# Performance work log

Hardware: AMD Instinct MI355X
Metric: run time of the kernel (lower is better)

The kernel has to match this reference:

```python
import jax, jax.numpy as jnp
import numpy as np

ALPHA = 4.0   # spikingjelly surrogate.Sigmoid default alpha
TAU = 2.0
HEADS = 8

@jax.custom_vjp
def spike_fn(x):
    return (x >= 0).astype(x.dtype)

def _spike_fwd(x):
    return spike_fn(x), x

def _spike_bwd(x, g):
    s = jax.nn.sigmoid(ALPHA * x)
    return (g * ALPHA * s * (1.0 - s),)

spike_fn.defvjp(_spike_fwd, _spike_bwd)

def lif(x, v_th=1.0):
    """Multi-step LIF over leading time axis. Hard reset to 0, detach_reset."""
    def step(v, xt):
        v = v + (xt - v) / TAU
        s = spike_fn(v - v_th)
        v = v * (1.0 - jax.lax.stop_gradient(s))
        return v, s
    _, spikes = jax.lax.scan(step, jnp.zeros_like(x[0]), x)
    return spikes

def conv1x1(x, w, b=None):
    # x: (T,B,C,H,W), w: (O,C) -> (T,B,O,H,W)
    y = jnp.einsum('tbchw,oc->tbohw', x, w)
    if b is not None:
        y = y + b[None, None, :, None, None]
    return y

def bn(x, gamma, beta, mean, var, eps=1e-5):
    inv = gamma / jnp.sqrt(var + eps)
    shift = beta - mean * inv
    return x * inv[None, None, :, None, None] + shift[None, None, :, None, None]

def setup_inputs() -> dict:
    key = jax.random.key(0)
    T, B, C, H, W = 4, 16, 512, 16, 16
    ks = jax.random.split(key, 24)
    def w(k):
        return jax.random.normal(k, (C, C), jnp.float32) * (1.0 / np.sqrt(C))
    def bn_params(k0, k1):
        g = 1.0 + 0.1 * jax.random.normal(k0, (C,), jnp.float32)
        b = 0.1 * jax.random.normal(k1, (C,), jnp.float32)
        m = 0.1 * jax.random.normal(jax.random.fold_in(k0, 7), (C,), jnp.float32)
        v = jax.random.uniform(jax.random.fold_in(k1, 7), (C,), jnp.float32, 0.5, 1.5)
        return g, b, m, v
    x = jax.random.normal(ks[0], (T, B, C, H, W), jnp.float32)
    q_g, q_b, q_m, q_v = bn_params(ks[4], ks[5])
    k_g, k_b, k_m, k_v = bn_params(ks[6], ks[7])
    v_g, v_b, v_m, v_v = bn_params(ks[8], ks[9])
    p_g, p_b2, p_m, p_v = bn_params(ks[10], ks[11])
    return {
        'x': x,
        'q_w': w(ks[1]), 'q_g': q_g, 'q_b': q_b, 'q_m': q_m, 'q_v': q_v,
        'k_w': w(ks[2]), 'k_g': k_g, 'k_b': k_b, 'k_m': k_m, 'k_v': k_v,
        'v_w': w(ks[3]), 'v_g': v_g, 'v_b': v_b, 'v_m': v_m, 'v_v': v_v,
        'proj_w': w(ks[12]),
        'proj_b': 0.1 * jax.random.normal(ks[13], (C,), jnp.float32),
        'p_g': p_g, 'p_b2': p_b2, 'p_m': p_m, 'p_v': p_v,
    }

def reference(x, q_w, q_g, q_b, q_m, q_v, k_w, k_g, k_b, k_m, k_v,
              v_w, v_g, v_b, v_m, v_v, proj_w, proj_b, p_g, p_b2, p_m, p_v):
    T, B, C, H, W = x.shape
    d = C // HEADS
    N = H * W
    identity = x
    xs = lif(x)  # shortcut_lif

    def to_heads(y):
        # (T,B,C,H,W) -> flatten(3) -> (T,B,C,N) -> (T,B,N,C) -> (T,B,N,h,d) -> (T,B,h,N,d)
        return y.reshape(T, B, C, N).transpose(0, 1, 3, 2).reshape(T, B, N, HEADS, d).transpose(0, 1, 3, 2, 4)

    q = to_heads(lif(bn(conv1x1(xs, q_w), q_g, q_b, q_m, q_v)))
    k = to_heads(lif(bn(conv1x1(xs, k_w), k_g, k_b, k_m, k_v)))
    v = to_heads(lif(bn(conv1x1(xs, v_w), v_g, v_b, v_m, v_v)))

    kv = (k * v).sum(axis=3, keepdims=True)        # (T,B,h,1,d) linear spike attention
    kv = lif(kv, v_th=0.5)                         # talking_heads_lif (conv1d never applied in source forward)
    attn = q * kv                                  # (T,B,h,N,d)

    y = attn.transpose(0, 1, 2, 4, 3).reshape(T, B, C, H, W)
    y = bn(conv1x1(y, proj_w, proj_b), p_g, p_b2, p_m, p_v)
    return y + identity
```

## Files before the change

kernel.cpp:

```cpp
#include <hip/hip_runtime.h>


#define T_  4
#define B_  16
#define C_  512
#define N_  256
#define O3_ 1536
#define EPS_ 1e-5f

typedef unsigned int uint32;

__global__ void k_prep(const float* __restrict__ qw, const float* __restrict__ kw,
                       const float* __restrict__ vw, const float* __restrict__ pw,
                       const float* qg,const float* qb,const float* qm,const float* qv,
                       const float* kg,const float* kb,const float* km,const float* kvr,
                       const float* vg,const float* vb,const float* vm,const float* vv,
                       const float* pg,const float* pb2,const float* pm,const float* pv,
                       const float* projb, const float* __restrict__ x,
                       float* __restrict__ wqkv_t, float* __restrict__ pwt,
                       float* __restrict__ bnc, uint32* __restrict__ xs_mask32,
                       uint32* __restrict__ cnt32){
    __shared__ float tile[64 * 65];
    __shared__ uint32 sm32[64 * 17];
    int bx = blockIdx.x, tid = threadIdx.x;
    if (bx < 256) {
        const float* src; float* dst; int ocol;
        int tl;
        if (bx < 192) { int g = bx / 64; tl = bx % 64;
            src = (g == 0) ? qw : (g == 1) ? kw : vw;
            dst = wqkv_t; ocol = g * 512;
        } else { tl = bx - 192; src = pw; dst = pwt; ocol = 0; }
        int o0 = (tl >> 3) * 64, c0 = (tl & 7) * 64;
        int dstride = (bx < 192) ? O3_ : C_;
        #pragma unroll
        for (int i = 0; i < 16; i++) {
            int idx = i * 256 + tid;
            int cl = idx & 63, ol = idx >> 6;
            tile[ol * 65 + cl] = src[(size_t)(o0 + ol) * C_ + c0 + cl];
        }
        __syncthreads();
        #pragma unroll
        for (int i = 0; i < 16; i++) {
            int idx = i * 256 + tid;
            int ol = idx & 63, cl = idx >> 6;
            dst[(size_t)(c0 + cl) * dstride + ocol + o0 + ol] = tile[ol * 65 + cl];
        }
    } else if (bx < 258) {
        int ch = (bx - 256) * 256 + tid;
        if (ch < C_) {
            {   float inv = qg[ch] / sqrtf(qv[ch] + EPS_);
                bnc[ch] = inv;            bnc[512 + ch]  = qb[ch] - qm[ch] * inv; }
            {   float inv = kg[ch] / sqrtf(kvr[ch] + EPS_);
                bnc[1024 + ch] = inv;     bnc[1536 + ch] = kb[ch] - km[ch] * inv; }
            {   float inv = vg[ch] / sqrtf(vv[ch] + EPS_);
                bnc[2048 + ch] = inv;     bnc[2560 + ch] = vb[ch] - vm[ch] * inv; }
            {   float inv = pg[ch] / sqrtf(pv[ch] + EPS_);
                float shift = pb2[ch] - pm[ch] * inv;
                bnc[3072 + ch] = inv;     bnc[3584 + ch] = projb[ch] * inv + shift; }
        }
    } else if (bx < 770) {
        int r = bx - 258;
        int b = r >> 5, rem = r & 31;
        int c0 = (rem >> 2) * 64, n0 = (rem & 3) * 64;
        #pragma unroll
        for (int i = 0; i < 4; i++) {
            int idx = i * 256 + tid;
            int nq = idx & 15, cl = idx >> 4;
            const float* xp = x + ((size_t)b * C_ + c0 + cl) * N_ + n0 + nq * 4;
            float4 xv[4];
            #pragma unroll
            for (int t = 0; t < 4; t++)
                xv[t] = *reinterpret_cast<const float4*>(xp + (size_t)t * B_ * C_ * N_);
            uint32 packed = 0;
            #pragma unroll
            for (int e = 0; e < 4; e++) {
                float v = 0.f; unsigned m = 0;
                #pragma unroll
                for (int t = 0; t < 4; t++) {
                    float xt = reinterpret_cast<const float*>(&xv[t])[e];
                    v = v + (xt - v) * 0.5f;
                    if (v - 1.0f >= 0.f) { m |= 1u << t; v = 0.f; }
                }
                packed |= m << (8 * e);
            }
            sm32[cl * 17 + nq] = packed;
        }
        __syncthreads();
        #pragma unroll
        for (int i = 0; i < 4; i++) {
            int idx = i * 256 + tid;
            int cq = idx & 15, nl = idx >> 4;
            uint32 outp = 0;
            #pragma unroll
            for (int e = 0; e < 4; e++) {
                uint32 wv = sm32[(cq * 4 + e) * 17 + (nl >> 2)];
                outp |= ((wv >> (8 * (nl & 3))) & 0xffu) << (8 * e);
            }
            xs_mask32[((size_t)b * N_ + n0 + nl) * 128 + (c0 >> 2) + cq] = outp;
        }
    } else {
        int idx = (bx - 770) * 256 + tid;
        cnt32[idx] = 0;
    }
}

__global__ __launch_bounds__(384) void
k2_qkv(const unsigned char* __restrict__ xs_mask,
       const float* __restrict__ wqkv_t,
       const float* __restrict__ bnc,
       unsigned char* __restrict__ q_mask,
       uint32* __restrict__ cnt32){
    __shared__ uint32 smask[128];
    __shared__ uint32 scnt;
    __shared__ uint32 slist[512];
    int n = blockIdx.x, b = blockIdx.y, tid = threadIdx.x;
    size_t colbase = ((size_t)b * N_ + n) * C_;
    if (tid < 128) smask[tid] = reinterpret_cast<const uint32*>(xs_mask + colbase)[tid];
    if (tid == 0) scnt = 0;
    __syncthreads();
    if (tid < 256) {
        const unsigned char* smb = (const unsigned char*)smask;
        #pragma unroll
        for (int h = 0; h < 2; h++) {
            int c = tid + (h << 8);
            unsigned m = smb[c];
            if (m) { unsigned p = atomicAdd(&scnt, 1u); slist[p] = (unsigned)c | (m << 16); }
        }
    }
    __syncthreads();
    int cnt = scnt;

    int g = tid >> 7;
    float acc[4][4];
    #pragma unroll
    for (int t = 0; t < 4; t++)
        #pragma unroll
        for (int i = 0; i < 4; i++) acc[t][i] = 0.f;

#define ACC4(t, w_) { acc[t][0]+=w_.x; acc[t][1]+=w_.y; acc[t][2]+=w_.z; acc[t][3]+=w_.w; }
    int j = 0;
    for (; j + 4 <= cnt; j += 4) {
        unsigned e0 = __builtin_amdgcn_readfirstlane(slist[j]);
        unsigned e1 = __builtin_amdgcn_readfirstlane(slist[j + 1]);
        unsigned e2 = __builtin_amdgcn_readfirstlane(slist[j + 2]);
        unsigned e3 = __builtin_amdgcn_readfirstlane(slist[j + 3]);
        float4 w0 = reinterpret_cast<const float4*>(wqkv_t + (size_t)(e0 & 0xffffu) * O3_)[tid];
        float4 w1 = reinterpret_cast<const float4*>(wqkv_t + (size_t)(e1 & 0xffffu) * O3_)[tid];
        float4 w2 = reinterpret_cast<const float4*>(wqkv_t + (size_t)(e2 & 0xffffu) * O3_)[tid];
        float4 w3 = reinterpret_cast<const float4*>(wqkv_t + (size_t)(e3 & 0xffffu) * O3_)[tid];
        unsigned m0 = e0 >> 16, m1 = e1 >> 16, m2 = e2 >> 16, m3 = e3 >> 16;
        if (m0 & 1u) ACC4(0, w0)  if (m0 & 2u) ACC4(1, w0)
        if (m0 & 4u) ACC4(2, w0)  if (m0 & 8u) ACC4(3, w0)
        if (m1 & 1u) ACC4(0, w1)  if (m1 & 2u) ACC4(1, w1)
        if (m1 & 4u) ACC4(2, w1)  if (m1 & 8u) ACC4(3, w1)
        if (m2 & 1u) ACC4(0, w2)  if (m2 & 2u) ACC4(1, w2)
        if (m2 & 4u) ACC4(2, w2)  if (m2 & 8u) ACC4(3, w2)
        if (m3 & 1u) ACC4(0, w3)  if (m3 & 2u) ACC4(1, w3)
        if (m3 & 4u) ACC4(2, w3)  if (m3 & 8u) ACC4(3, w3)
    }
    for (; j < cnt; j++) {
        unsigned e0 = __builtin_amdgcn_readfirstlane(slist[j]);
        float4 w0 = reinterpret_cast<const float4*>(wqkv_t + (size_t)(e0 & 0xffffu) * O3_)[tid];
        unsigned m0 = e0 >> 16;
        if (m0 & 1u) ACC4(0, w0)  if (m0 & 2u) ACC4(1, w0)
        if (m0 & 4u) ACC4(2, w0)  if (m0 & 8u) ACC4(3, w0)
    }
#undef ACC4

    int chb = (tid & 127) * 4;
    unsigned packed = 0;
    #pragma unroll
    for (int i = 0; i < 4; i++) {
        int ch = chb + i;
        float inv = bnc[g * 1024 + ch];
        float sh  = bnc[g * 1024 + 512 + ch];
        float v = 0.f; unsigned bits = 0;
        #pragma unroll
        for (int t = 0; t < 4; t++) {
            float pre = acc[t][i] * inv + sh;
            v = v + (pre - v) * 0.5f;
            if (v - 1.0f >= 0.f) { bits |= 1u << t; v = 0.f; }
        }
        packed |= bits << (8 * i);
    }
    if (g == 0)      reinterpret_cast<uint32*>(q_mask + colbase)[tid] = packed;
    else if (g == 1) smask[tid - 128] = packed;
    __syncthreads();
    if (g == 2) {
        unsigned kb = smask[tid - 256];
        unsigned kv = packed & kb;
        if (kv) {
            uint32* cbase = cnt32 + b * 1024 + (chb >> 1);
            #pragma unroll
            for (int t = 0; t < 4; t++) {
                unsigned v01 = ((kv >> t) & 1u) | (((kv >> (8 + t)) & 1u) << 16);
                unsigned v23 = ((kv >> (16 + t)) & 1u) | (((kv >> (24 + t)) & 1u) << 16);
                if (v01) atomicAdd(cbase + t * 256, v01);
                if (v23) atomicAdd(cbase + t * 256 + 1, v23);
            }
        }
    }
}

__global__ __launch_bounds__(256) void
k4_attn_proj(const unsigned char* __restrict__ q_mask,
             const uint32* __restrict__ cnt32,
             const float* __restrict__ pwt,
             const float* __restrict__ bnc,
             float* __restrict__ y_t){
    __shared__ uint32 smask[2][128];
    __shared__ uint32 scnt[2];
    __shared__ uint32 slist[2][512];
    int b = blockIdx.y, tid = threadIdx.x;
    int col = tid >> 7, ctid = tid & 127;
    int n = blockIdx.x * 2 + col;
    size_t colbase = ((size_t)b * N_ + n) * C_;
    unsigned kvs_packed = 0;
    {
        const uint32* cbase = cnt32 + b * 1024 + ctid * 2;
        uint32 c01[4], c23[4];
        #pragma unroll
        for (int t = 0; t < 4; t++) { c01[t] = cbase[t * 256]; c23[t] = cbase[t * 256 + 1]; }
        #pragma unroll
        for (int e = 0; e < 4; e++) {
            float v = 0.f; unsigned bits = 0;
            #pragma unroll
            for (int t = 0; t < 4; t++) {
                uint32 pair = (e < 2) ? c01[t] : c23[t];
                float cn = (float)(int)((e & 1) ? (pair >> 16) : (pair & 0xffffu));
                v = v + (cn - v) * 0.5f;
                if (v - 0.5f >= 0.f) { bits |= 1u << t; v = 0.f; }
            }
            kvs_packed |= bits << (8 * e);
        }
    }
    {
        uint32 qm = reinterpret_cast<const uint32*>(q_mask + colbase)[ctid];
        smask[col][ctid] = qm & kvs_packed;
    }
    if (ctid == 0) scnt[col] = 0;
    __syncthreads();
    {
        const unsigned char* smb = (const unsigned char*)smask[col];
        #pragma unroll
        for (int h = 0; h < 4; h++) {
            int c = ctid * 4 + h;
            unsigned m = smb[c];
            if (m) { unsigned p = atomicAdd(&scnt[col], 1u); slist[col][p] = (unsigned)c | (m << 16); }
        }
    }
    __syncthreads();
    int cnt = scnt[col];
    const uint32* lst = slist[col];

    float acc[4][4];
    #pragma unroll
    for (int t = 0; t < 4; t++)
        #pragma unroll
        for (int i = 0; i < 4; i++) acc[t][i] = 0.f;

#define ACC4(t, w_) { acc[t][0]+=w_.x; acc[t][1]+=w_.y; acc[t][2]+=w_.z; acc[t][3]+=w_.w; }
    int j = 0;
    for (; j + 4 <= cnt; j += 4) {
        unsigned e0 = __builtin_amdgcn_readfirstlane(lst[j]);
        unsigned e1 = __builtin_amdgcn_readfirstlane(lst[j + 1]);
        unsigned e2 = __builtin_amdgcn_readfirstlane(lst[j + 2]);
        unsigned e3 = __builtin_amdgcn_readfirstlane(lst[j + 3]);
        float4 w0 = reinterpret_cast<const float4*>(pwt + (size_t)(e0 & 0xffffu) * C_)[ctid];
        float4 w1 = reinterpret_cast<const float4*>(pwt + (size_t)(e1 & 0xffffu) * C_)[ctid];
        float4 w2 = reinterpret_cast<const float4*>(pwt + (size_t)(e2 & 0xffffu) * C_)[ctid];
        float4 w3 = reinterpret_cast<const float4*>(pwt + (size_t)(e3 & 0xffffu) * C_)[ctid];
        unsigned m0 = e0 >> 16, m1 = e1 >> 16, m2 = e2 >> 16, m3 = e3 >> 16;
        if (m0 & 1u) ACC4(0, w0)  if (m0 & 2u) ACC4(1, w0)
        if (m0 & 4u) ACC4(2, w0)  if (m0 & 8u) ACC4(3, w0)
        if (m1 & 1u) ACC4(0, w1)  if (m1 & 2u) ACC4(1, w1)
        if (m1 & 4u) ACC4(2, w1)  if (m1 & 8u) ACC4(3, w1)
        if (m2 & 1u) ACC4(0, w2)  if (m2 & 2u) ACC4(1, w2)
        if (m2 & 4u) ACC4(2, w2)  if (m2 & 8u) ACC4(3, w2)
        if (m3 & 1u) ACC4(0, w3)  if (m3 & 2u) ACC4(1, w3)
        if (m3 & 4u) ACC4(2, w3)  if (m3 & 8u) ACC4(3, w3)
    }
    for (; j < cnt; j++) {
        unsigned e0 = __builtin_amdgcn_readfirstlane(lst[j]);
        float4 w0 = reinterpret_cast<const float4*>(pwt + (size_t)(e0 & 0xffffu) * C_)[ctid];
        unsigned m0 = e0 >> 16;
        if (m0 & 1u) ACC4(0, w0)  if (m0 & 2u) ACC4(1, w0)
        if (m0 & 4u) ACC4(2, w0)  if (m0 & 8u) ACC4(3, w0)
    }
#undef ACC4

    float4 inv = reinterpret_cast<const float4*>(bnc + 3072)[ctid];
    float4 sh  = reinterpret_cast<const float4*>(bnc + 3584)[ctid];
    #pragma unroll
    for (int t = 0; t < 4; t++) {
        float4 y4;
        y4.x = acc[t][0] * inv.x + sh.x;
        y4.y = acc[t][1] * inv.y + sh.y;
        y4.z = acc[t][2] * inv.z + sh.z;
        y4.w = acc[t][3] * inv.w + sh.w;
        reinterpret_cast<float4*>(y_t + (((size_t)t * B_ + b) * N_ + n) * C_)[ctid] = y4;
    }
}

__global__ void k5_out(const float* __restrict__ y_t, const float* __restrict__ x,
                       float* __restrict__ out){
    __shared__ float tile[64 * 65];
    int b = blockIdx.x, o0 = blockIdx.y * 64, n0 = blockIdx.z * 64;
    int tid = threadIdx.x;
    for (int t = 0; t < T_; t++) {
        __syncthreads();
        #pragma unroll
        for (int i = 0; i < 4; i++) {
            int idx = i * 256 + tid;
            int o4 = idx & 15, nl = idx >> 4;
            float4 yv = *reinterpret_cast<const float4*>(
                y_t + (((size_t)t * B_ + b) * N_ + n0 + nl) * C_ + o0 + o4 * 4);
            tile[(o4 * 4 + 0) * 65 + nl] = yv.x;
            tile[(o4 * 4 + 1) * 65 + nl] = yv.y;
            tile[(o4 * 4 + 2) * 65 + nl] = yv.z;
            tile[(o4 * 4 + 3) * 65 + nl] = yv.w;
        }
        __syncthreads();
        #pragma unroll
        for (int i = 0; i < 4; i++) {
            int idx = i * 256 + tid;
            int n4 = idx & 15, ol = idx >> 4;
            size_t a = (((size_t)t * B_ + b) * C_ + o0 + ol) * N_ + n0 + n4 * 4;
            float4 xv = *reinterpret_cast<const float4*>(x + a);
            float4 yv;
            yv.x = tile[ol * 65 + n4 * 4 + 0] + xv.x;
            yv.y = tile[ol * 65 + n4 * 4 + 1] + xv.y;
            yv.z = tile[ol * 65 + n4 * 4 + 2] + xv.z;
            yv.w = tile[ol * 65 + n4 * 4 + 3] + xv.w;
            *reinterpret_cast<float4*>(out + a) = yv;
        }
    }
}

extern "C" void kernel_launch(void* const* d_in, const int* in_sizes, int n_in,
                              void* d_out, int out_size, void* d_ws, size_t ws_size,
                              hipStream_t stream){
    const float* x     = (const float*)d_in[0];
    const float* q_w   = (const float*)d_in[1];
    const float* q_g   = (const float*)d_in[2];
    const float* q_b   = (const float*)d_in[3];
    const float* q_m   = (const float*)d_in[4];
    const float* q_v   = (const float*)d_in[5];
    const float* k_w   = (const float*)d_in[6];
    const float* k_g   = (const float*)d_in[7];
    const float* k_b   = (const float*)d_in[8];
    const float* k_m   = (const float*)d_in[9];
    const float* k_v   = (const float*)d_in[10];
    const float* v_w   = (const float*)d_in[11];
    const float* v_g   = (const float*)d_in[12];
    const float* v_b   = (const float*)d_in[13];
    const float* v_m   = (const float*)d_in[14];
    const float* v_v   = (const float*)d_in[15];
    const float* pr_w  = (const float*)d_in[16];
    const float* pr_b  = (const float*)d_in[17];
    const float* p_g   = (const float*)d_in[18];
    const float* p_b2  = (const float*)d_in[19];
    const float* p_m   = (const float*)d_in[20];
    const float* p_v   = (const float*)d_in[21];
    float* out = (float*)d_out;

    char* ws = (char*)d_ws;
    float* wqkv_t          = (float*)(ws + 0);
    float* pwt             = (float*)(ws + 3145728);
    float* bnc             = (float*)(ws + 4194304);
    unsigned char* xs_mask = (unsigned char*)(ws + 4210688);
    unsigned char* q_mask  = (unsigned char*)(ws + 6307840);
    uint32* cnt32          = (uint32*)(ws + 8404992);
    float* y_t             = (float*)(ws + 8421376);

    hipLaunchKernelGGL(k_prep, dim3(786), dim3(256), 0, stream,
                       q_w, k_w, v_w, pr_w,
                       q_g,q_b,q_m,q_v, k_g,k_b,k_m,k_v, v_g,v_b,v_m,v_v,
                       p_g,p_b2,p_m,p_v, pr_b, x,
                       wqkv_t, pwt, bnc, (uint32*)xs_mask, cnt32);
    hipLaunchKernelGGL(k2_qkv, dim3(N_, B_), dim3(384), 0, stream,
                       xs_mask, wqkv_t, bnc, q_mask, cnt32);
    hipLaunchKernelGGL(k4_attn_proj, dim3(N_/2, B_), dim3(256), 0, stream,
                       q_mask, cnt32, pwt, bnc, y_t);
    hipLaunchKernelGGL(k5_out, dim3(B_, C_/64, N_/64), dim3(256), 0, stream, y_t, x, out);
}
```

Baseline: 202.1 us.

## Split sparse weight-gather reduction across two thread halves in qkv and proj kernels

Doubles the block size of the QKV and projection kernels so that two thread groups each walk half of the active-channel list, then combine partial accumulators through shared memory before the LIF/BN epilogue. This aims to cut the serial length of the gather-accumulate loop per block and expose more memory-level parallelism. In exchange it adds a large shared-memory buffer, an extra barrier and reduction step, and lowers how many blocks fit per CU.

```diff
diff --git a/kernel.cpp b/kernel.cpp
--- a/kernel.cpp
+++ b/kernel.cpp
@@ -104,7 +104,7 @@
     }
 }
 
-__global__ __launch_bounds__(384) void
+__global__ __launch_bounds__(768) void
 k2_qkv(const unsigned char* __restrict__ xs_mask,
        const float* __restrict__ wqkv_t,
        const float* __restrict__ bnc,
@@ -113,7 +113,10 @@
     __shared__ uint32 smask[128];
     __shared__ uint32 scnt;
     __shared__ uint32 slist[512];
+    __shared__ float  sacc[384 * 16];
     int n = blockIdx.x, b = blockIdx.y, tid = threadIdx.x;
+    int half = (tid >= 384);
+    int ltid = half ? tid - 384 : tid;
     size_t colbase = ((size_t)b * N_ + n) * C_;
     if (tid < 128) smask[tid] = reinterpret_cast<const uint32*>(xs_mask + colbase)[tid];
     if (tid == 0) scnt = 0;
@@ -129,8 +132,11 @@
     }
     __syncthreads();
     int cnt = scnt;
-
-    int g = tid >> 7;
+    int mid = (cnt >> 1) & ~3;
+    int jbeg = half ? mid : 0;
+    int jend = half ? cnt : mid;
+
+    int g = ltid >> 7;
     float acc[4][4];
     #pragma unroll
     for (int t = 0; t < 4; t++)
@@ -138,16 +144,16 @@
         for (int i = 0; i < 4; i++) acc[t][i] = 0.f;
 
 #define ACC4(t, w_) { acc[t][0]+=w_.x; acc[t][1]+=w_.y; acc[t][2]+=w_.z; acc[t][3]+=w_.w; }
-    int j = 0;
-    for (; j + 4 <= cnt; j += 4) {
+    int j = jbeg;
+    for (; j + 4 <= jend; j += 4) {
         unsigned e0 = __builtin_amdgcn_readfirstlane(slist[j]);
         unsigned e1 = __builtin_amdgcn_readfirstlane(slist[j + 1]);
         unsigned e2 = __builtin_amdgcn_readfirstlane(slist[j + 2]);
         unsigned e3 = __builtin_amdgcn_readfirstlane(slist[j + 3]);
-        float4 w0 = reinterpret_cast<const float4*>(wqkv_t + (size_t)(e0 & 0xffffu) * O3_)[tid];
-        float4 w1 = reinterpret_cast<const float4*>(wqkv_t + (size_t)(e1 & 0xffffu) * O3_)[tid];
-        float4 w2 = reinterpret_cast<const float4*>(wqkv_t + (size_t)(e2 & 0xffffu) * O3_)[tid];
-        float4 w3 = reinterpret_cast<const float4*>(wqkv_t + (size_t)(e3 & 0xffffu) * O3_)[tid];
+        float4 w0 = reinterpret_cast<const float4*>(wqkv_t + (size_t)(e0 & 0xffffu) * O3_)[ltid];
+        float4 w1 = reinterpret_cast<const float4*>(wqkv_t + (size_t)(e1 & 0xffffu) * O3_)[ltid];
+        float4 w2 = reinterpret_cast<const float4*>(wqkv_t + (size_t)(e2 & 0xffffu) * O3_)[ltid];
+        float4 w3 = reinterpret_cast<const float4*>(wqkv_t + (size_t)(e3 & 0xffffu) * O3_)[ltid];
         unsigned m0 = e0 >> 16, m1 = e1 >> 16, m2 = e2 >> 16, m3 = e3 >> 16;
         if (m0 & 1u) ACC4(0, w0)  if (m0 & 2u) ACC4(1, w0)
         if (m0 & 4u) ACC4(2, w0)  if (m0 & 8u) ACC4(3, w0)
@@ -158,36 +164,52 @@
         if (m3 & 1u) ACC4(0, w3)  if (m3 & 2u) ACC4(1, w3)
         if (m3 & 4u) ACC4(2, w3)  if (m3 & 8u) ACC4(3, w3)
     }
-    for (; j < cnt; j++) {
+    for (; j < jend; j++) {
         unsigned e0 = __builtin_amdgcn_readfirstlane(slist[j]);
-        float4 w0 = reinterpret_cast<const float4*>(wqkv_t + (size_t)(e0 & 0xffffu) * O3_)[tid];
+        float4 w0 = reinterpret_cast<const float4*>(wqkv_t + (size_t)(e0 & 0xffffu) * O3_)[ltid];
         unsigned m0 = e0 >> 16;
         if (m0 & 1u) ACC4(0, w0)  if (m0 & 2u) ACC4(1, w0)
         if (m0 & 4u) ACC4(2, w0)  if (m0 & 8u) ACC4(3, w0)
     }
 #undef ACC4
 
-    int chb = (tid & 127) * 4;
+    if (half) {
+        #pragma unroll
+        for (int t = 0; t < 4; t++)
+            #pragma unroll
+            for (int i = 0; i < 4; i++) sacc[ltid * 16 + t * 4 + i] = acc[t][i];
+    }
+    __syncthreads();
+    if (!half) {
+        #pragma unroll
+        for (int t = 0; t < 4; t++)
+            #pragma unroll
+            for (int i = 0; i < 4; i++) acc[t][i] += sacc[ltid * 16 + t * 4 + i];
+    }
+
+    int chb = (ltid & 127) * 4;
     unsigned packed = 0;
-    #pragma unroll
-    for (int i = 0; i < 4; i++) {
-        int ch = chb + i;
-        float inv = bnc[g * 1024 + ch];
-        float sh  = bnc[g * 1024 + 512 + ch];
-        float v = 0.f; unsigned bits = 0;
-        #pragma unroll
-        for (int t = 0; t < 4; t++) {
-            float pre = acc[t][i] * inv + sh;
-            v = v + (pre - v) * 0.5f;
-            if (v - 1.0f >= 0.f) { bits |= 1u << t; v = 0.f; }
-        }
-        packed |= bits << (8 * i);
-    }
-    if (g == 0)      reinterpret_cast<uint32*>(q_mask + colbase)[tid] = packed;
-    else if (g == 1) smask[tid - 128] = packed;
-    __syncthreads();
-    if (g == 2) {
-        unsigned kb = smask[tid - 256];
+    if (!half) {
+        #pragma unroll
+        for (int i = 0; i < 4; i++) {
+            int ch = chb + i;
+            float inv = bnc[g * 1024 + ch];
+            float sh  = bnc[g * 1024 + 512 + ch];
+            float v = 0.f; unsigned bits = 0;
+            #pragma unroll
+            for (int t = 0; t < 4; t++) {
+                float pre = acc[t][i] * inv + sh;
+                v = v + (pre - v) * 0.5f;
+                if (v - 1.0f >= 0.f) { bits |= 1u << t; v = 0.f; }
+            }
+            packed |= bits << (8 * i);
+        }
+        if (g == 0)      reinterpret_cast<uint32*>(q_mask + colbase)[ltid] = packed;
+        else if (g == 1) smask[ltid - 128] = packed;
+    }
+    __syncthreads();
+    if (!half && g == 2) {
+        unsigned kb = smask[ltid - 256];
         unsigned kv = packed & kb;
         if (kv) {
             uint32* cbase = cnt32 + b * 1024 + (chb >> 1);
@@ -202,7 +224,7 @@
     }
 }
 
-__global__ __launch_bounds__(256) void
+__global__ __launch_bounds__(512) void
 k4_attn_proj(const unsigned char* __restrict__ q_mask,
              const uint32* __restrict__ cnt32,
              const float* __restrict__ pwt,
@@ -211,12 +233,13 @@
     __shared__ uint32 smask[2][128];
     __shared__ uint32 scnt[2];
     __shared__ uint32 slist[2][512];
+    __shared__ float  sacc[256 * 16];
     int b = blockIdx.y, tid = threadIdx.x;
-    int col = tid >> 7, ctid = tid & 127;
+    int half = tid >> 8, col = (tid >> 7) & 1, ctid = tid & 127;
     int n = blockIdx.x * 2 + col;
     size_t colbase = ((size_t)b * N_ + n) * C_;
-    unsigned kvs_packed = 0;
-    {
+    if (!half) {
+        unsigned kvs_packed = 0;
         const uint32* cbase = cnt32 + b * 1024 + ctid * 2;
         uint32 c01[4], c23[4];
         #pragma unroll
@@ -233,14 +256,12 @@
             }
             kvs_packed |= bits << (8 * e);
         }
-    }
-    {
         uint32 qm = reinterpret_cast<const uint32*>(q_mask + colbase)[ctid];
         smask[col][ctid] = qm & kvs_packed;
-    }
-    if (ctid == 0) scnt[col] = 0;
-    __syncthreads();
-    {
+        if (ctid == 0) scnt[col] = 0;
+    }
+    __syncthreads();
+    if (!half) {
         const unsigned char* smb = (const unsigned char*)smask[col];
         #pragma unroll
         for (int h = 0; h < 4; h++) {
@@ -252,6 +273,9 @@
     __syncthreads();
     int cnt = scnt[col];
     const uint32* lst = slist[col];
+    int mid = (cnt >> 1) & ~3;
+    int jbeg = half ? mid : 0;
+    int jend = half ? cnt : mid;
 
     float acc[4][4];
     #pragma unroll
@@ -260,8 +284,8 @@
         for (int i = 0; i < 4; i++) acc[t][i] = 0.f;
 
 #define ACC4(t, w_) { acc[t][0]+=w_.x; acc[t][1]+=w_.y; acc[t][2]+=w_.z; acc[t][3]+=w_.w; }
-    int j = 0;
-    for (; j + 4 <= cnt; j += 4) {
+    int j = jbeg;
+    for (; j + 4 <= jend; j += 4) {
         unsigned e0 = __builtin_amdgcn_readfirstlane(lst[j]);
         unsigned e1 = __builtin_amdgcn_readfirstlane(lst[j + 1]);
         unsigned e2 = __builtin_amdgcn_readfirstlane(lst[j + 2]);
@@ -280,7 +304,7 @@
         if (m3 & 1u) ACC4(0, w3)  if (m3 & 2u) ACC4(1, w3)
         if (m3 & 4u) ACC4(2, w3)  if (m3 & 8u) ACC4(3, w3)
     }
-    for (; j < cnt; j++) {
+    for (; j < jend; j++) {
         unsigned e0 = __builtin_amdgcn_readfirstlane(lst[j]);
         float4 w0 = reinterpret_cast<const float4*>(pwt + (size_t)(e0 & 0xffffu) * C_)[ctid];
         unsigned m0 = e0 >> 16;
@@ -289,16 +313,31 @@
     }
 #undef ACC4
 
-    float4 inv = reinterpret_cast<const float4*>(bnc + 3072)[ctid];
-    float4 sh  = reinterpret_cast<const float4*>(bnc + 3584)[ctid];
-    #pragma unroll
-    for (int t = 0; t < 4; t++) {
-        float4 y4;
-        y4.x = acc[t][0] * inv.x + sh.x;
-        y4.y = acc[t][1] * inv.y + sh.y;
-        y4.z = acc[t][2] * inv.z + sh.z;
-        y4.w = acc[t][3] * inv.w + sh.w;
-        reinterpret_cast<float4*>(y_t + (((size_t)t * B_ + b) * N_ + n) * C_)[ctid] = y4;
+    int slot = col * 128 + ctid;
+    if (half) {
+        #pragma unroll
+        for (int t = 0; t < 4; t++)
+            #pragma unroll
+            for (int i = 0; i < 4; i++) sacc[slot * 16 + t * 4 + i] = acc[t][i];
+    }
+    __syncthreads();
+    if (!half) {
+        #pragma unroll
+        for (int t = 0; t < 4; t++)
+            #pragma unroll
+            for (int i = 0; i < 4; i++) acc[t][i] += sacc[slot * 16 + t * 4 + i];
+
+        float4 inv = reinterpret_cast<const float4*>(bnc + 3072)[ctid];
+        float4 sh  = reinterpret_cast<const float4*>(bnc + 3584)[ctid];
+        #pragma unroll
+        for (int t = 0; t < 4; t++) {
+            float4 y4;
+            y4.x = acc[t][0] * inv.x + sh.x;
+            y4.y = acc[t][1] * inv.y + sh.y;
+            y4.z = acc[t][2] * inv.z + sh.z;
+            y4.w = acc[t][3] * inv.w + sh.w;
+            reinterpret_cast<float4*>(y_t + (((size_t)t * B_ + b) * N_ + n) * C_)[ctid] = y4;
+        }
     }
 }
 
@@ -378,9 +417,9 @@
                        q_g,q_b,q_m,q_v, k_g,k_b,k_m,k_v, v_g,v_b,v_m,v_v,
                        p_g,p_b2,p_m,p_v, pr_b, x,
                        wqkv_t, pwt, bnc, (uint32*)xs_mask, cnt32);
-    hipLaunchKernelGGL(k2_qkv, dim3(N_, B_), dim3(384), 0, stream,
+    hipLaunchKernelGGL(k2_qkv, dim3(N_, B_), dim3(768), 0, stream,
                        xs_mask, wqkv_t, bnc, q_mask, cnt32);
-    hipLaunchKernelGGL(k4_attn_proj, dim3(N_/2, B_), dim3(256), 0, stream,
+    hipLaunchKernelGGL(k4_attn_proj, dim3(N_/2, B_), dim3(512), 0, stream,
                        q_mask, cnt32, pwt, bnc, y_t);
     hipLaunchKernelGGL(k5_out, dim3(B_, C_/64, N_/64), dim3(256), 0, stream, y_t, x, out);
 }
```

After: 207.8 us. 1.03x slower.
